# Kernel optimization log

Measured on AMD Instinct MI355X. Metric: run time of the kernel, lower is better.

Reference implementation:

```python
import jax, jax.numpy as jnp
import numpy as np

LN_EPS = 1e-5

def setup_inputs() -> dict:
    key = jax.random.key(0)
    B, T, D, H, NB = 32, 384, 512, 16, 5  # NB = 5 MHSA blocks actually used
    ks = jax.random.split(key, 10)
    s = 1.0 / np.sqrt(D)
    def w(k, shape):
        return jax.random.normal(k, shape, jnp.float32) * s
    return {
        "x": jax.random.normal(ks[0], (B, T, D), jnp.float32),
        # stacked params for the 5 used MHSA blocks, order:
        # [tmp_attn, layer1_1, layer1_2, layer1_3, layer2_1]
        "qw": w(ks[1], (NB, D, D)), "qb": w(ks[2], (NB, D)),
        "kw": w(ks[3], (NB, D, D)), "kb": w(ks[4], (NB, D)),
        "vw": w(ks[5], (NB, D, D)), "vb": w(ks[6], (NB, D)),
        "temp": jnp.ones((NB, H, 1, 1), jnp.float32),
        "ln_g": jnp.ones((D,), jnp.float32),
        "ln_b": jnp.zeros((D,), jnp.float32),
        "fus_w": w(ks[7], (D, D)), "fus_b": w(ks[8], (D,)),
        "num_heads": H,
    }


def _mhsa(x, wq, bq, wk, bk, wv, bv, temp, H):
    # Faithful to torch: .view(B, H, D//H, T) is a flat reshape of (B,T,D).
    B, T, D = x.shape
    d = D // H
    q = (x @ wq.T + bq).reshape(B, H, d, T)
    k = (x @ wk.T + bk).reshape(B, H, d, T)
    v = (x @ wv.T + bv).reshape(B, H, d, T)
    # k^T @ v -> (B,H,T,T), scaled by per-head temperature, softmax over last dim
    attn = jax.nn.softmax(jnp.einsum("bhdt,bhds->bhts", k, v) * temp, axis=-1)
    out = jnp.einsum("bhdt,bhts->bhds", q, attn)  # (B,H,d,T)
    return out.reshape(B, T, D)


def _layernorm(x, g, b):
    mu = jnp.mean(x, axis=-1, keepdims=True)
    var = jnp.mean(jnp.square(x - mu), axis=-1, keepdims=True)
    return (x - mu) * jax.lax.rsqrt(var + LN_EPS) * g + b


def reference(x, qw, qb, kw, kb, vw, vb, temp, ln_g, ln_b, fus_w, fus_b, num_heads):
    H = num_heads
    blk = lambda i, z: _mhsa(z, qw[i], qb[i], kw[i], kb[i], vw[i], vb[i], temp[i], H)
    x_ = blk(0, x)
    c1, c2, c3 = jnp.split(x, 3, axis=1)
    tmp_layer1 = jnp.concatenate([blk(1, c1), blk(2, c2), blk(3, c3)], axis=1) + x_
    tmp_layer2 = blk(4, _layernorm(tmp_layer1, ln_g, ln_b)) + x_
    alpha = jnp.stack([tmp_layer1, tmp_layer2], axis=0)  # (2,B,T,D)
    alpha = alpha @ fus_w.T + fus_b
    alpha = jax.nn.softmax(alpha, axis=0)
    return tmp_layer1 * alpha[0] + tmp_layer2 * alpha[1]
```

## Files before the change

kernel.cpp:

```cpp
#include <hip/hip_runtime.h>

typedef __attribute__((ext_vector_type(8))) _Float16 half8;
typedef __attribute__((ext_vector_type(4))) _Float16 half4v;
typedef __attribute__((ext_vector_type(2))) _Float16 half2v;
typedef __attribute__((ext_vector_type(4))) float float4v;

__device__ __forceinline__ float4v mfma16x16x32_f16(half8 a, half8 b, float4v c) {
#if defined(__HIP_DEVICE_COMPILE__)
#if __has_builtin(__builtin_amdgcn_mfma_f32_16x16x32_f16)
  return __builtin_amdgcn_mfma_f32_16x16x32_f16(a, b, c, 0, 0, 0);
#elif __has_builtin(__builtin_amdgcn_mfma_f32_16x16x32f16)
  return __builtin_amdgcn_mfma_f32_16x16x32f16(a, b, c, 0, 0, 0);
#else
#error "no 16x16x32 f16 mfma"
#endif
#else
  (void)a; (void)b;
  return c;
#endif
}

__device__ __forceinline__ float4v mfma16x16x16_f16(half4v a, half4v b, float4v c) {
#if defined(__HIP_DEVICE_COMPILE__)
#if __has_builtin(__builtin_amdgcn_mfma_f32_16x16x16f16)
  return __builtin_amdgcn_mfma_f32_16x16x16f16(a, b, c, 0, 0, 0);
#elif __has_builtin(__builtin_amdgcn_mfma_f32_16x16x16_f16)
  return __builtin_amdgcn_mfma_f32_16x16x16_f16(a, b, c, 0, 0, 0);
#else
#error "no 16x16x16 f16 mfma"
#endif
#else
  (void)a; (void)b;
  return c;
#endif
}

__device__ __forceinline__ void gl_lds16(const unsigned short* g, unsigned short* l) {
#if defined(__HIP_DEVICE_COMPILE__)
#if __has_builtin(__builtin_amdgcn_global_load_lds)
  __builtin_amdgcn_global_load_lds(
      (const __attribute__((address_space(1))) unsigned int*)g,
      (__attribute__((address_space(3))) unsigned int*)l, 16, 0, 0);
#else
  *(uint4*)l = *(const uint4*)g;
#endif
#else
  (void)g; (void)l;
#endif
}

__device__ __forceinline__ float fexp2(float x) {
#if defined(__HIP_DEVICE_COMPILE__)
#if __has_builtin(__builtin_amdgcn_exp2f)
  return __builtin_amdgcn_exp2f(x);
#else
  return __expf(x * 0.6931471805599453f);
#endif
#else
  return x;
#endif
}

__device__ __forceinline__ half2v pk_f16(float a, float b) {
#if defined(__HIP_DEVICE_COMPILE__)
#if __has_builtin(__builtin_amdgcn_cvt_pkrtz)
  return __builtin_bit_cast(half2v, __builtin_amdgcn_cvt_pkrtz(a, b));
#else
  half2v r;
  r[0] = (_Float16)a;
  r[1] = (_Float16)b;
  return r;
#endif
#else
  half2v r;
  r[0] = (_Float16)a;
  r[1] = (_Float16)b;
  return r;
#endif
}

__device__ __forceinline__ unsigned short f2h(float f) {
  union { _Float16 h; unsigned short u; } v;
  v.h = (_Float16)f;
  return v.u;
}

__global__ __launch_bounds__(256) void cvt_f32_f16(const float* __restrict__ in,
                                                   unsigned short* __restrict__ out, int n4) {
  int i = blockIdx.x * 256 + threadIdx.x;
  if (i >= n4) return;
  float4 v = ((const float4*)in)[i];
  uint2 o;
  o.x = (unsigned)f2h(v.x) | ((unsigned)f2h(v.y) << 16);
  o.y = (unsigned)f2h(v.z) | ((unsigned)f2h(v.w) << 16);
  ((uint2*)out)[i] = o;
}

#define GEMM_CORE(WGPTR)                                                               \
  for (int k0 = 0; k0 < 512; k0 += 64) {                                               \
    _Pragma("unroll") for (int rnd = 0; rnd < 4; ++rnd) {                              \
      const int slot = rnd * 512 + tid;                                                \
      const int r = slot >> 3;                                                         \
      const int c = (slot & 7) ^ (r & 7);                                              \
      const size_t src = ((r >> 7) ? xrow1 : xrow0) + (size_t)(r & 127) * 512 +        \
                         (size_t)(k0 + c * 8);                                         \
      gl_lds16(Xbase + src, &Xs[slot * 8]);                                            \
    }                                                                                  \
    _Pragma("unroll") for (int rnd = 0; rnd < 2; ++rnd) {                              \
      const int s2 = rnd * 512 + tid;                                                  \
      const int r = s2 >> 3;                                                           \
      const int c = (s2 & 7) ^ (r & 7);                                                \
      gl_lds16((WGPTR) + (size_t)r * 512 + k0 + c * 8, &Wt[s2 * 8]);                   \
    }                                                                                  \
    __syncthreads();                                                                   \
    _Pragma("unroll") for (int kk = 0; kk < 2; ++kk) {                                 \
      half8 af[4], bf[4];                                                              \
      const int ch = ((kk * 4 + grp) ^ (col & 7)) * 8;                                 \
      _Pragma("unroll") for (int i = 0; i < 4; ++i)                                    \
          af[i] = *(const half8*)&Xs[(wm + i * 16 + col) * 64 + ch];                   \
      _Pragma("unroll") for (int j = 0; j < 4; ++j)                                    \
          bf[j] = *(const half8*)&Wt[(wn + j * 16 + col) * 64 + ch];                   \
      _Pragma("unroll") for (int i = 0; i < 4; ++i)                                    \
          _Pragma("unroll") for (int j = 0; j < 4; ++j)                                \
              acc[i][j] = mfma16x16x32_f16(af[i], bf[j], acc[i][j]);                   \
    }                                                                                  \
    __syncthreads();                                                                   \
  }

__global__ __launch_bounds__(512) void gemm_qkv(
    const unsigned short* __restrict__ X,
    const unsigned short* __restrict__ Wq, const unsigned short* __restrict__ Wk,
    const unsigned short* __restrict__ Wv,
    const float* __restrict__ bq, const float* __restrict__ bk, const float* __restrict__ bv,
    unsigned short* __restrict__ Cq, unsigned short* __restrict__ Ck, unsigned short* __restrict__ Cv,
    int wsel_mode, int widx_fixed) {
  const int nt = blockIdx.x, mt = blockIdx.y, z = blockIdx.z;
  const unsigned short* W = (z == 0) ? Wq : ((z == 1) ? Wk : Wv);
  const float* bias = (z == 0) ? bq : ((z == 1) ? bk : bv);
  unsigned short* C = (z == 0) ? Cq : ((z == 1) ? Ck : Cv);
  const int cpart = mt % 3, bb = (mt / 3) * 2;
  const int widx = wsel_mode ? (1 + cpart) : widx_fixed;
  W += (size_t)widx * 512 * 512;
  bias += widx * 512;

  const size_t grow0 = (size_t)bb * 384 + cpart * 128;
  const size_t grow1 = grow0 + 384;
  const size_t xrow0 = grow0 * 512, xrow1 = grow1 * 512;
  const unsigned short* Xbase = X;

  __shared__ __align__(16) unsigned short Xs[2048 * 8];
  __shared__ __align__(16) unsigned short Wt[1024 * 8];
  const int tid = threadIdx.x, lane = tid & 63, w = tid >> 6;
  const int col = lane & 15, grp = lane >> 4;
  const int wm = (w >> 1) * 64, wn = (w & 1) * 64;

  const float4v zero4 = {0.f, 0.f, 0.f, 0.f};
  float4v acc[4][4];
#pragma unroll
  for (int i = 0; i < 4; ++i)
#pragma unroll
    for (int j = 0; j < 4; ++j) acc[i][j] = zero4;

  GEMM_CORE(W + (size_t)nt * 128 * 512)

#pragma unroll
  for (int j = 0; j < 4; ++j) {
    const int n = nt * 128 + wn + j * 16 + col;
    const float bj = bias[n];
#pragma unroll
    for (int i = 0; i < 4; ++i)
#pragma unroll
      for (int r = 0; r < 4; ++r) {
        const int m = wm + i * 16 + grp * 4 + r;
        const size_t grow = ((m >> 7) ? grow1 : grow0) + (m & 127);
        C[grow * 512 + n] = f2h(acc[i][j][r] + bj);
      }
  }
}

__global__ __launch_bounds__(512) void gemm_fusion(
    const unsigned short* __restrict__ X, const unsigned short* __restrict__ Wf,
    const float* __restrict__ tl1, const float* __restrict__ tl2, float* __restrict__ outp) {
  const int nt = blockIdx.x, mt = blockIdx.y;
  const size_t grow0 = (size_t)mt * 256, grow1 = grow0 + 128;
  const size_t xrow0 = grow0 * 512, xrow1 = grow1 * 512;
  const unsigned short* Xbase = X;

  __shared__ __align__(16) unsigned short Xs[2048 * 8];
  __shared__ __align__(16) unsigned short Wt[1024 * 8];
  const int tid = threadIdx.x, lane = tid & 63, w = tid >> 6;
  const int col = lane & 15, grp = lane >> 4;
  const int wm = (w >> 1) * 64, wn = (w & 1) * 64;

  const float4v zero4 = {0.f, 0.f, 0.f, 0.f};
  float4v acc[4][4];
#pragma unroll
  for (int i = 0; i < 4; ++i)
#pragma unroll
    for (int j = 0; j < 4; ++j) acc[i][j] = zero4;

  GEMM_CORE(Wf + (size_t)nt * 128 * 512)

#pragma unroll
  for (int j = 0; j < 4; ++j) {
    const int n = nt * 128 + wn + j * 16 + col;
#pragma unroll
    for (int i = 0; i < 4; ++i)
#pragma unroll
      for (int r = 0; r < 4; ++r) {
        const int m = wm + i * 16 + grp * 4 + r;
        const size_t off = (((m >> 7) ? grow1 : grow0) + (m & 127)) * 512 + n;
        const float t1 = tl1[off], t2 = tl2[off];
        const float sg = 1.0f / (1.0f + __expf(-acc[i][j][r]));
        outp[off] = t2 + (t1 - t2) * sg;
      }
  }
}

template <int T, int NB>
__global__ __launch_bounds__(512) void attn_kernel(
    const unsigned short* __restrict__ Qb, const unsigned short* __restrict__ Kb,
    const unsigned short* __restrict__ Vb, const float* __restrict__ temp_base,
    const float* add_src,
    float* outp, int chunk_elems,
    const float* __restrict__ tl1_src, unsigned short* __restrict__ diff_out) {
  constexpr int NT = T / 16;
  constexpr int NSW = (T / 16) / 8;
  constexpr int SLAB = T * 32;
  const int h = blockIdx.x, b = blockIdx.y, cb = blockIdx.z;
  const int base = b * (384 * 512) + cb * chunk_elems + h * SLAB;
  const float tl2e = temp_base[cb * 16 + h] * 1.4426950408889634f;

  __shared__ __align__(16) unsigned short KVt[T][40];
  __shared__ __align__(16) float Zp[2][NB][8][16];

  const int tid = threadIdx.x, lane = tid & 63, w = tid >> 6;
  const int col = lane & 15, grp = lane >> 4;

  auto stage = [&](const unsigned short* src) {
    constexpr int ITER = (T * 4) / 512;
#pragma unroll
    for (int p = 0; p < ITER; ++p) {
      const int f = p * 512 + tid;
      const int t = f >> 2, blk = (f & 3) * 8;
      unsigned short tmp[8];
#pragma unroll
      for (int i = 0; i < 8; ++i) tmp[i] = src[(size_t)(blk + i) * T + t];
      *(uint4*)&KVt[t][blk] = *(const uint4*)tmp;
    }
  };

  stage(Vb + base);
  __syncthreads();
  half8 vfr[NSW];
#pragma unroll
  for (int si = 0; si < NSW; ++si)
    vfr[si] = *(const half8*)&KVt[(w + si * 8) * 16 + col][grp * 8];
  __syncthreads();
  stage(Kb + base);
  __syncthreads();

  const float4v zero4 = {0.f, 0.f, 0.f, 0.f};
  const unsigned short* Qsl = Qb + base;
  float4v oacc[NSW][2];
#pragma unroll
  for (int si = 0; si < NSW; ++si) {
    oacc[si][0] = zero4;
    oacc[si][1] = zero4;
  }

  for (int g = 0; g < NT / NB; ++g) {
    const int par = g & 1;
    float pe[NB][NSW][4];
#pragma unroll
    for (int u = 0; u < NB; ++u) {
      const int tt = g * NB + u;
      half8 kf = *(const half8*)&KVt[tt * 16 + col][grp * 8];
      float z0 = 0.f, z1 = 0.f, z2 = 0.f, z3 = 0.f;
#pragma unroll
      for (int si = 0; si < NSW; ++si) {
        float4v s = mfma16x16x32_f16(kf, vfr[si], zero4);
        pe[u][si][0] = fexp2(s[0] * tl2e);
        pe[u][si][1] = fexp2(s[1] * tl2e);
        pe[u][si][2] = fexp2(s[2] * tl2e);
        pe[u][si][3] = fexp2(s[3] * tl2e);
        z0 += pe[u][si][0];
        z1 += pe[u][si][1];
        z2 += pe[u][si][2];
        z3 += pe[u][si][3];
      }
#pragma unroll
      for (int m = 1; m < 16; m <<= 1) {
        z0 += __shfl_xor(z0, m);
        z1 += __shfl_xor(z1, m);
        z2 += __shfl_xor(z2, m);
        z3 += __shfl_xor(z3, m);
      }
      if (col == 0) {
        float4v zv = {z0, z1, z2, z3};
        *(float4v*)&Zp[par][u][w][grp * 4] = zv;
      }
    }
    half4v qa[NB][2];
#pragma unroll
    for (int u = 0; u < NB; ++u) {
      const int toff = (g * NB + u) * 16 + grp * 4;
      qa[u][0] = *(const half4v*)(Qsl + col * T + toff);
      qa[u][1] = *(const half4v*)(Qsl + (16 + col) * T + toff);
    }
    __syncthreads();
#pragma unroll
    for (int u = 0; u < NB; ++u) {
      float4v zs = zero4;
#pragma unroll
      for (int ww = 0; ww < 8; ++ww) zs += *(const float4v*)&Zp[par][u][ww][grp * 4];
      const float zi0 = 1.0f / zs[0], zi1 = 1.0f / zs[1], zi2 = 1.0f / zs[2],
                  zi3 = 1.0f / zs[3];
#pragma unroll
      for (int si = 0; si < NSW; ++si) {
        half2v lo = pk_f16(pe[u][si][0] * zi0, pe[u][si][1] * zi1);
        half2v hi = pk_f16(pe[u][si][2] * zi2, pe[u][si][3] * zi3);
        half4v pb = __builtin_shufflevector(lo, hi, 0, 1, 2, 3);
        oacc[si][0] = mfma16x16x16_f16(qa[u][0], pb, oacc[si][0]);
        oacc[si][1] = mfma16x16x16_f16(qa[u][1], pb, oacc[si][1]);
      }
    }
  }

#pragma unroll
  for (int si = 0; si < NSW; ++si) {
    const int s = (w + si * 8) * 16 + col;
#pragma unroll
    for (int m0 = 0; m0 < 2; ++m0) {
#pragma unroll
      for (int r = 0; r < 4; ++r) {
        const int dd = m0 * 16 + grp * 4 + r;
        const int off = base + dd * T + s;
        float v = oacc[si][m0][r];
        if (add_src) v += add_src[off];
        outp[off] = v;
        if (diff_out) diff_out[off] = f2h(tl1_src[off] - v);
      }
    }
  }
}

__global__ __launch_bounds__(256) void ln_kernel(const float* __restrict__ xin,
                                                 const float* __restrict__ g,
                                                 const float* __restrict__ bb,
                                                 unsigned short* __restrict__ y) {
  const int row = blockIdx.x * 4 + (threadIdx.x >> 6);
  const int lane = threadIdx.x & 63;
  const float* xr = xin + (size_t)row * 512;
  float4 v0 = *(const float4*)&xr[lane * 8];
  float4 v1 = *(const float4*)&xr[lane * 8 + 4];
  float s = v0.x + v0.y + v0.z + v0.w + v1.x + v1.y + v1.z + v1.w;
  float q = v0.x * v0.x + v0.y * v0.y + v0.z * v0.z + v0.w * v0.w +
            v1.x * v1.x + v1.y * v1.y + v1.z * v1.z + v1.w * v1.w;
#pragma unroll
  for (int m = 1; m < 64; m <<= 1) {
    s += __shfl_xor(s, m);
    q += __shfl_xor(q, m);
  }
  const float mean = s * (1.0f / 512.0f);
  const float var = q * (1.0f / 512.0f) - mean * mean;
  const float rs = rsqrtf(var + 1e-5f);
  float4 g0 = *(const float4*)&g[lane * 8];
  float4 g1 = *(const float4*)&g[lane * 8 + 4];
  float4 b0 = *(const float4*)&bb[lane * 8];
  float4 b1 = *(const float4*)&bb[lane * 8 + 4];
  uint4 o;
  o.x = (unsigned)f2h((v0.x - mean) * rs * g0.x + b0.x) |
        ((unsigned)f2h((v0.y - mean) * rs * g0.y + b0.y) << 16);
  o.y = (unsigned)f2h((v0.z - mean) * rs * g0.z + b0.z) |
        ((unsigned)f2h((v0.w - mean) * rs * g0.w + b0.w) << 16);
  o.z = (unsigned)f2h((v1.x - mean) * rs * g1.x + b1.x) |
        ((unsigned)f2h((v1.y - mean) * rs * g1.y + b1.y) << 16);
  o.w = (unsigned)f2h((v1.z - mean) * rs * g1.z + b1.z) |
        ((unsigned)f2h((v1.w - mean) * rs * g1.w + b1.w) << 16);
  *(uint4*)&y[(size_t)row * 512 + lane * 8] = o;
}

extern "C" void kernel_launch(void* const* d_in, const int* in_sizes, int n_in,
                              void* d_out, int out_size, void* d_ws, size_t ws_size,
                              hipStream_t stream) {
  const float* x = (const float*)d_in[0];
  const float* qw = (const float*)d_in[1];
  const float* qb = (const float*)d_in[2];
  const float* kw = (const float*)d_in[3];
  const float* kb = (const float*)d_in[4];
  const float* vw = (const float*)d_in[5];
  const float* vb = (const float*)d_in[6];
  const float* temp = (const float*)d_in[7];
  const float* ln_g = (const float*)d_in[8];
  const float* ln_b = (const float*)d_in[9];
  const float* fus_w = (const float*)d_in[10];
  float* out = (float*)d_out;

  const size_t NE = (size_t)32 * 384 * 512;
  const size_t WE = (size_t)5 * 512 * 512;

  char* p = (char*)d_ws;
  auto alloc = [&](size_t bytes) {
    char* r = p;
    p += (bytes + 255) & ~(size_t)255;
    return r;
  };
  unsigned short* xb = (unsigned short*)alloc(NE * 2);
  unsigned short* wqb = (unsigned short*)alloc(WE * 2);
  unsigned short* wkb = (unsigned short*)alloc(WE * 2);
  unsigned short* wvb = (unsigned short*)alloc(WE * 2);
  unsigned short* fwb = (unsigned short*)alloc((size_t)512 * 512 * 2);
  unsigned short* Qb = (unsigned short*)alloc(NE * 2);
  unsigned short* Kb = (unsigned short*)alloc(NE * 2);
  unsigned short* Vb = (unsigned short*)alloc(NE * 2);
  float* xres = (float*)alloc(NE * 4);
  float* tl1 = (float*)alloc(NE * 4);
  unsigned short* yb = (unsigned short*)alloc(NE * 2);

  cvt_f32_f16<<<(int)((NE / 4 + 255) / 256), 256, 0, stream>>>(x, xb, (int)(NE / 4));
  cvt_f32_f16<<<(int)((WE / 4 + 255) / 256), 256, 0, stream>>>(qw, wqb, (int)(WE / 4));
  cvt_f32_f16<<<(int)((WE / 4 + 255) / 256), 256, 0, stream>>>(kw, wkb, (int)(WE / 4));
  cvt_f32_f16<<<(int)((WE / 4 + 255) / 256), 256, 0, stream>>>(vw, wvb, (int)(WE / 4));
  cvt_f32_f16<<<256, 256, 0, stream>>>(fus_w, fwb, 512 * 512 / 4);

  gemm_qkv<<<dim3(4, 48, 3), 512, 0, stream>>>(xb, wqb, wkb, wvb, qb, kb, vb, Qb, Kb, Vb, 0, 0);
  attn_kernel<384, 4><<<dim3(16, 32, 1), 512, 0, stream>>>(Qb, Kb, Vb, temp, nullptr, xres, 0,
                                                           nullptr, nullptr);
  gemm_qkv<<<dim3(4, 48, 3), 512, 0, stream>>>(xb, wqb, wkb, wvb, qb, kb, vb, Qb, Kb, Vb, 1, 0);
  attn_kernel<128, 2><<<dim3(16, 32, 3), 512, 0, stream>>>(Qb, Kb, Vb, temp + 16, xres, tl1,
                                                           128 * 512, nullptr, nullptr);
  ln_kernel<<<12288 / 4, 256, 0, stream>>>(tl1, ln_g, ln_b, yb);
  gemm_qkv<<<dim3(4, 48, 3), 512, 0, stream>>>(yb, wqb, wkb, wvb, qb, kb, vb, Qb, Kb, Vb, 0, 4);
  attn_kernel<384, 4><<<dim3(16, 32, 1), 512, 0, stream>>>(Qb, Kb, Vb, temp + 64, xres, xres, 0,
                                                           tl1, yb);
  gemm_fusion<<<dim3(4, 48), 512, 0, stream>>>(yb, fwb, tl1, xres, out);

  (void)in_sizes; (void)n_in; (void)out_size; (void)ws_size;
}
```

Measured before the change: 416.4 us.

## Merge independent QKV GEMMs and attention launches, fuse residual add into layernorm

Merges the five conversion launches into one kernel, computes both first-stage QKV projections in a single 6-z GEMM launch, and runs the block-0 and chunked attention in one merged launch with output buffers aliased into yb and out. The residual add moves out of the chunked attention into the layernorm kernel. V fragments now load straight from global memory instead of being staged through LDS, and the row sums use DPP reductions. The aim is fewer launches, more blocks in flight and fewer LDS round trips. The cost is more complex buffer aliasing and an extra fp32 diff buffer written by the tail attention.

```diff
diff --git a/kernel.cpp b/kernel.cpp
--- a/kernel.cpp
+++ b/kernel.cpp
@@ -85,15 +85,53 @@
   return v.u;
 }
 
-__global__ __launch_bounds__(256) void cvt_f32_f16(const float* __restrict__ in,
-                                                   unsigned short* __restrict__ out, int n4) {
-  int i = blockIdx.x * 256 + threadIdx.x;
-  if (i >= n4) return;
-  float4 v = ((const float4*)in)[i];
+__device__ __forceinline__ float row_sum16(float x) {
+#if defined(__HIP_DEVICE_COMPILE__)
+#if __has_builtin(__builtin_amdgcn_update_dpp)
+  int v;
+  v = __builtin_bit_cast(int, x);
+  x += __builtin_bit_cast(float, __builtin_amdgcn_update_dpp(0, v, 0x128, 0xF, 0xF, true));
+  v = __builtin_bit_cast(int, x);
+  x += __builtin_bit_cast(float, __builtin_amdgcn_update_dpp(0, v, 0x124, 0xF, 0xF, true));
+  v = __builtin_bit_cast(int, x);
+  x += __builtin_bit_cast(float, __builtin_amdgcn_update_dpp(0, v, 0x122, 0xF, 0xF, true));
+  v = __builtin_bit_cast(int, x);
+  x += __builtin_bit_cast(float, __builtin_amdgcn_update_dpp(0, v, 0x121, 0xF, 0xF, true));
+  return x;
+#else
+  x += __shfl_xor(x, 1);
+  x += __shfl_xor(x, 2);
+  x += __shfl_xor(x, 4);
+  x += __shfl_xor(x, 8);
+  return x;
+#endif
+#else
+  return x;
+#endif
+}
+
+__global__ __launch_bounds__(256) void cvt_multi(
+    const float* __restrict__ s0, unsigned short* __restrict__ d0, int n0,
+    const float* __restrict__ s1, unsigned short* __restrict__ d1,
+    const float* __restrict__ s2, unsigned short* __restrict__ d2,
+    const float* __restrict__ s3, unsigned short* __restrict__ d3, int n13,
+    const float* __restrict__ s4, unsigned short* __restrict__ d4, int n4c) {
+  const int y = blockIdx.y;
+  const float* s;
+  unsigned short* d;
+  int n;
+  if (y == 0) { s = s0; d = d0; n = n0; }
+  else if (y == 1) { s = s1; d = d1; n = n13; }
+  else if (y == 2) { s = s2; d = d2; n = n13; }
+  else if (y == 3) { s = s3; d = d3; n = n13; }
+  else { s = s4; d = d4; n = n4c; }
+  const int i = blockIdx.x * 256 + threadIdx.x;
+  if (i >= n) return;
+  float4 v = ((const float4*)s)[i];
   uint2 o;
   o.x = (unsigned)f2h(v.x) | ((unsigned)f2h(v.y) << 16);
   o.y = (unsigned)f2h(v.z) | ((unsigned)f2h(v.w) << 16);
-  ((uint2*)out)[i] = o;
+  ((uint2*)d)[i] = o;
 }
 
 #define GEMM_CORE(WGPTR)                                                               \
@@ -127,19 +165,23 @@
     __syncthreads();                                                                   \
   }
 
-__global__ __launch_bounds__(512) void gemm_qkv(
+__global__ __launch_bounds__(512) void gemm_qkv6(
     const unsigned short* __restrict__ X,
     const unsigned short* __restrict__ Wq, const unsigned short* __restrict__ Wk,
     const unsigned short* __restrict__ Wv,
     const float* __restrict__ bq, const float* __restrict__ bk, const float* __restrict__ bv,
-    unsigned short* __restrict__ Cq, unsigned short* __restrict__ Ck, unsigned short* __restrict__ Cv,
-    int wsel_mode, int widx_fixed) {
+    unsigned short* __restrict__ CqA, unsigned short* __restrict__ CkA,
+    unsigned short* __restrict__ CvA, unsigned short* __restrict__ CqB,
+    unsigned short* __restrict__ CkB, unsigned short* __restrict__ CvB,
+    int widx_fixed) {
   const int nt = blockIdx.x, mt = blockIdx.y, z = blockIdx.z;
-  const unsigned short* W = (z == 0) ? Wq : ((z == 1) ? Wk : Wv);
-  const float* bias = (z == 0) ? bq : ((z == 1) ? bk : bv);
-  unsigned short* C = (z == 0) ? Cq : ((z == 1) ? Ck : Cv);
+  const int zz = z % 3, mode = z / 3;
+  const unsigned short* W = (zz == 0) ? Wq : ((zz == 1) ? Wk : Wv);
+  const float* bias = (zz == 0) ? bq : ((zz == 1) ? bk : bv);
+  unsigned short* C = mode ? ((zz == 0) ? CqB : ((zz == 1) ? CkB : CvB))
+                           : ((zz == 0) ? CqA : ((zz == 1) ? CkA : CvA));
   const int cpart = mt % 3, bb = (mt / 3) * 2;
-  const int widx = wsel_mode ? (1 + cpart) : widx_fixed;
+  const int widx = mode ? (1 + cpart) : widx_fixed;
   W += (size_t)widx * 512 * 512;
   bias += widx * 512;
 
@@ -180,7 +222,7 @@
 
 __global__ __launch_bounds__(512) void gemm_fusion(
     const unsigned short* __restrict__ X, const unsigned short* __restrict__ Wf,
-    const float* __restrict__ tl1, const float* __restrict__ tl2, float* __restrict__ outp) {
+    const float* __restrict__ dif, const float* __restrict__ tl2, float* __restrict__ outp) {
   const int nt = blockIdx.x, mt = blockIdx.y;
   const size_t grow0 = (size_t)mt * 256, grow1 = grow0 + 128;
   const size_t xrow0 = grow0 * 512, xrow1 = grow1 * 512;
@@ -210,34 +252,33 @@
       for (int r = 0; r < 4; ++r) {
         const int m = wm + i * 16 + grp * 4 + r;
         const size_t off = (((m >> 7) ? grow1 : grow0) + (m & 127)) * 512 + n;
-        const float t1 = tl1[off], t2 = tl2[off];
+        const float d = dif[off], t2 = tl2[off];
         const float sg = 1.0f / (1.0f + __expf(-acc[i][j][r]));
-        outp[off] = t2 + (t1 - t2) * sg;
+        outp[off] = t2 + d * sg;
       }
   }
 }
 
 template <int T, int NB>
-__global__ __launch_bounds__(512) void attn_kernel(
+__device__ __forceinline__ void attn_body(
     const unsigned short* __restrict__ Qb, const unsigned short* __restrict__ Kb,
     const unsigned short* __restrict__ Vb, const float* __restrict__ temp_base,
     const float* add_src,
-    float* outp, int chunk_elems,
-    const float* __restrict__ tl1_src, unsigned short* __restrict__ diff_out) {
+    float* outp, int chunk_elems, int cb, int h, int b,
+    const float* tl1_src,
+    unsigned short* diff16, float* diff32,
+    unsigned short* KVt, float* Zpf) {
   constexpr int NT = T / 16;
-  constexpr int NSW = (T / 16) / 8;
+  constexpr int NSW = NT / 8;
   constexpr int SLAB = T * 32;
-  const int h = blockIdx.x, b = blockIdx.y, cb = blockIdx.z;
   const int base = b * (384 * 512) + cb * chunk_elems + h * SLAB;
   const float tl2e = temp_base[cb * 16 + h] * 1.4426950408889634f;
 
-  __shared__ __align__(16) unsigned short KVt[T][40];
-  __shared__ __align__(16) float Zp[2][NB][8][16];
-
   const int tid = threadIdx.x, lane = tid & 63, w = tid >> 6;
   const int col = lane & 15, grp = lane >> 4;
 
-  auto stage = [&](const unsigned short* src) {
+  {
+    const unsigned short* src = Kb + base;
     constexpr int ITER = (T * 4) / 512;
 #pragma unroll
     for (int p = 0; p < ITER; ++p) {
@@ -246,18 +287,21 @@
       unsigned short tmp[8];
 #pragma unroll
       for (int i = 0; i < 8; ++i) tmp[i] = src[(size_t)(blk + i) * T + t];
-      *(uint4*)&KVt[t][blk] = *(const uint4*)tmp;
+      *(uint4*)&KVt[t * 40 + blk] = *(const uint4*)tmp;
     }
-  };
-
-  stage(Vb + base);
-  __syncthreads();
+  }
   half8 vfr[NSW];
-#pragma unroll
-  for (int si = 0; si < NSW; ++si)
-    vfr[si] = *(const half8*)&KVt[(w + si * 8) * 16 + col][grp * 8];
-  __syncthreads();
-  stage(Kb + base);
+  {
+    const unsigned short* Vg = Vb + base;
+#pragma unroll
+    for (int si = 0; si < NSW; ++si) {
+      const int s = (w + si * 8) * 16 + col;
+      union { unsigned short u[8]; half8 v; } t8;
+#pragma unroll
+      for (int i = 0; i < 8; ++i) t8.u[i] = Vg[(size_t)(grp * 8 + i) * T + s];
+      vfr[si] = t8.v;
+    }
+  }
   __syncthreads();
 
   const float4v zero4 = {0.f, 0.f, 0.f, 0.f};
@@ -275,30 +319,27 @@
 #pragma unroll
     for (int u = 0; u < NB; ++u) {
       const int tt = g * NB + u;
-      half8 kf = *(const half8*)&KVt[tt * 16 + col][grp * 8];
+      half8 kf = *(const half8*)&KVt[(tt * 16 + col) * 40 + grp * 8];
       float z0 = 0.f, z1 = 0.f, z2 = 0.f, z3 = 0.f;
 #pragma unroll
       for (int si = 0; si < NSW; ++si) {
-        float4v s = mfma16x16x32_f16(kf, vfr[si], zero4);
-        pe[u][si][0] = fexp2(s[0] * tl2e);
-        pe[u][si][1] = fexp2(s[1] * tl2e);
-        pe[u][si][2] = fexp2(s[2] * tl2e);
-        pe[u][si][3] = fexp2(s[3] * tl2e);
+        float4v sv = mfma16x16x32_f16(kf, vfr[si], zero4);
+        pe[u][si][0] = fexp2(sv[0] * tl2e);
+        pe[u][si][1] = fexp2(sv[1] * tl2e);
+        pe[u][si][2] = fexp2(sv[2] * tl2e);
+        pe[u][si][3] = fexp2(sv[3] * tl2e);
         z0 += pe[u][si][0];
         z1 += pe[u][si][1];
         z2 += pe[u][si][2];
         z3 += pe[u][si][3];
       }
-#pragma unroll
-      for (int m = 1; m < 16; m <<= 1) {
-        z0 += __shfl_xor(z0, m);
-        z1 += __shfl_xor(z1, m);
-        z2 += __shfl_xor(z2, m);
-        z3 += __shfl_xor(z3, m);
-      }
+      z0 = row_sum16(z0);
+      z1 = row_sum16(z1);
+      z2 = row_sum16(z2);
+      z3 = row_sum16(z3);
       if (col == 0) {
         float4v zv = {z0, z1, z2, z3};
-        *(float4v*)&Zp[par][u][w][grp * 4] = zv;
+        *(float4v*)&Zpf[((par * NB + u) * 8 + w) * 16 + grp * 4] = zv;
       }
     }
     half4v qa[NB][2];
@@ -313,7 +354,8 @@
     for (int u = 0; u < NB; ++u) {
       float4v zs = zero4;
 #pragma unroll
-      for (int ww = 0; ww < 8; ++ww) zs += *(const float4v*)&Zp[par][u][ww][grp * 4];
+      for (int ww = 0; ww < 8; ++ww)
+        zs += *(const float4v*)&Zpf[((par * NB + u) * 8 + ww) * 16 + grp * 4];
       const float zi0 = 1.0f / zs[0], zi1 = 1.0f / zs[1], zi2 = 1.0f / zs[2],
                   zi3 = 1.0f / zs[3];
 #pragma unroll
@@ -336,24 +378,65 @@
       for (int r = 0; r < 4; ++r) {
         const int dd = m0 * 16 + grp * 4 + r;
         const int off = base + dd * T + s;
-        float v = oacc[si][m0][r];
+        const float o = oacc[si][m0][r];
+        float v = o;
         if (add_src) v += add_src[off];
+        if (tl1_src) {
+          const float d = tl1_src[off] - o;
+          diff16[off] = f2h(d);
+          diff32[off] = d;
+        }
         outp[off] = v;
-        if (diff_out) diff_out[off] = f2h(tl1_src[off] - v);
       }
     }
   }
 }
 
-__global__ __launch_bounds__(256) void ln_kernel(const float* __restrict__ xin,
+__global__ __launch_bounds__(512, 8) void attn_merged(
+    const unsigned short* __restrict__ Q0, const unsigned short* __restrict__ K0,
+    const unsigned short* __restrict__ V0, const unsigned short* __restrict__ Qc,
+    const unsigned short* __restrict__ Kc, const unsigned short* __restrict__ Vc,
+    const float* __restrict__ temp, float* xres, float* tl1) {
+  __shared__ __align__(16) unsigned short Ks[384 * 40];
+  __shared__ __align__(16) float Zp[2 * 4 * 8 * 16];
+  const int id = blockIdx.x + 16 * (blockIdx.y + 32 * blockIdx.z);
+  const int part = id & 3, rest = id >> 2;
+  const int h = rest & 15, b = rest >> 4;
+  if (part == 0)
+    attn_body<384, 4>(Q0, K0, V0, temp, nullptr, xres, 0, 0, h, b,
+                      nullptr, nullptr, nullptr, Ks, Zp);
+  else
+    attn_body<128, 2>(Qc, Kc, Vc, temp + 16, nullptr, tl1, 128 * 512, part - 1, h, b,
+                      nullptr, nullptr, nullptr, Ks, Zp);
+}
+
+__global__ __launch_bounds__(512) void attn_tail(
+    const unsigned short* __restrict__ Q, const unsigned short* __restrict__ K,
+    const unsigned short* __restrict__ V, const float* __restrict__ temp4,
+    const float* add_src, float* tl12, unsigned short* __restrict__ diff16,
+    float* diff32) {
+  __shared__ __align__(16) unsigned short Ks[384 * 40];
+  __shared__ __align__(16) float Zp[2 * 4 * 8 * 16];
+  attn_body<384, 4>(Q, K, V, temp4, add_src, tl12, 0, 0, blockIdx.x, blockIdx.y,
+                    tl12, diff16, diff32, Ks, Zp);
+}
+
+__global__ __launch_bounds__(256) void ln_kernel(const float* __restrict__ a,
+                                                 const float* __restrict__ c,
                                                  const float* __restrict__ g,
                                                  const float* __restrict__ bb,
                                                  unsigned short* __restrict__ y) {
   const int row = blockIdx.x * 4 + (threadIdx.x >> 6);
   const int lane = threadIdx.x & 63;
-  const float* xr = xin + (size_t)row * 512;
-  float4 v0 = *(const float4*)&xr[lane * 8];
-  float4 v1 = *(const float4*)&xr[lane * 8 + 4];
+  const float* ar = a + (size_t)row * 512;
+  const float* cr = c + (size_t)row * 512;
+  float4 a0 = *(const float4*)&ar[lane * 8];
+  float4 a1 = *(const float4*)&ar[lane * 8 + 4];
+  float4 c0 = *(const float4*)&cr[lane * 8];
+  float4 c1 = *(const float4*)&cr[lane * 8 + 4];
+  float4 v0, v1;
+  v0.x = a0.x + c0.x; v0.y = a0.y + c0.y; v0.z = a0.z + c0.z; v0.w = a0.w + c0.w;
+  v1.x = a1.x + c1.x; v1.y = a1.y + c1.y; v1.z = a1.z + c1.z; v1.w = a1.w + c1.w;
   float s = v0.x + v0.y + v0.z + v0.w + v1.x + v1.y + v1.z + v1.w;
   float q = v0.x * v0.x + v0.y * v0.y + v0.z * v0.z + v0.w * v0.w +
             v1.x * v1.x + v1.y * v1.y + v1.z * v1.z + v1.w * v1.w;
@@ -418,23 +501,24 @@
   float* tl1 = (float*)alloc(NE * 4);
   unsigned short* yb = (unsigned short*)alloc(NE * 2);
 
-  cvt_f32_f16<<<(int)((NE / 4 + 255) / 256), 256, 0, stream>>>(x, xb, (int)(NE / 4));
-  cvt_f32_f16<<<(int)((WE / 4 + 255) / 256), 256, 0, stream>>>(qw, wqb, (int)(WE / 4));
-  cvt_f32_f16<<<(int)((WE / 4 + 255) / 256), 256, 0, stream>>>(kw, wkb, (int)(WE / 4));
-  cvt_f32_f16<<<(int)((WE / 4 + 255) / 256), 256, 0, stream>>>(vw, wvb, (int)(WE / 4));
-  cvt_f32_f16<<<256, 256, 0, stream>>>(fus_w, fwb, 512 * 512 / 4);
-
-  gemm_qkv<<<dim3(4, 48, 3), 512, 0, stream>>>(xb, wqb, wkb, wvb, qb, kb, vb, Qb, Kb, Vb, 0, 0);
-  attn_kernel<384, 4><<<dim3(16, 32, 1), 512, 0, stream>>>(Qb, Kb, Vb, temp, nullptr, xres, 0,
-                                                           nullptr, nullptr);
-  gemm_qkv<<<dim3(4, 48, 3), 512, 0, stream>>>(xb, wqb, wkb, wvb, qb, kb, vb, Qb, Kb, Vb, 1, 0);
-  attn_kernel<128, 2><<<dim3(16, 32, 3), 512, 0, stream>>>(Qb, Kb, Vb, temp + 16, xres, tl1,
-                                                           128 * 512, nullptr, nullptr);
-  ln_kernel<<<12288 / 4, 256, 0, stream>>>(tl1, ln_g, ln_b, yb);
-  gemm_qkv<<<dim3(4, 48, 3), 512, 0, stream>>>(yb, wqb, wkb, wvb, qb, kb, vb, Qb, Kb, Vb, 0, 4);
-  attn_kernel<384, 4><<<dim3(16, 32, 1), 512, 0, stream>>>(Qb, Kb, Vb, temp + 64, xres, xres, 0,
-                                                           tl1, yb);
-  gemm_fusion<<<dim3(4, 48), 512, 0, stream>>>(yb, fwb, tl1, xres, out);
+  unsigned short* Qc = yb;
+  unsigned short* Kc = (unsigned short*)out;
+  unsigned short* Vc = Kc + NE;
+
+  cvt_multi<<<dim3((int)(NE / 4 / 256), 5), 256, 0, stream>>>(
+      x, xb, (int)(NE / 4), qw, wqb, kw, wkb, vw, wvb, (int)(WE / 4), fus_w, fwb,
+      512 * 512 / 4);
+
+  gemm_qkv6<<<dim3(4, 48, 6), 512, 0, stream>>>(xb, wqb, wkb, wvb, qb, kb, vb,
+                                                Qb, Kb, Vb, Qc, Kc, Vc, 0);
+  attn_merged<<<dim3(16, 32, 4), 512, 0, stream>>>(Qb, Kb, Vb, Qc, Kc, Vc, temp,
+                                                   xres, tl1);
+  ln_kernel<<<12288 / 4, 256, 0, stream>>>(tl1, xres, ln_g, ln_b, yb);
+  gemm_qkv6<<<dim3(4, 48, 3), 512, 0, stream>>>(yb, wqb, wkb, wvb, qb, kb, vb,
+                                                Qb, Kb, Vb, Qb, Kb, Vb, 4);
+  attn_tail<<<dim3(16, 32, 1), 512, 0, stream>>>(Qb, Kb, Vb, temp + 64, xres, tl1,
+                                                 yb, xres);
+  gemm_fusion<<<dim3(4, 48), 512, 0, stream>>>(yb, fwb, xres, tl1, out);
 
   (void)in_sizes; (void)n_in; (void)out_size; (void)ws_size;
 }
```

New measurement: 750.0 us. 1.8x slower.
